# Performance work log

Hardware: AMD Instinct MI355X
Metric: run time of the kernel (lower is better)

Reference implementation:

```python
import jax, jax.numpy as jnp
import numpy as np

H = 128; W = 128; WH = 8; WW = 8; SH = 4; SW = 4
DIM = 512; HEADS = 16; HD = DIM // HEADS; HIDDEN = 2048
NH = H // WH; NW = W // WW; NWIN = NH * NW; WL = WH * WW
EPS = 1e-5
SCALE = HD ** -0.5


def _rel_pos_index():
    # Swin-style relative position index, static (WL, WL) int table
    coords = np.stack(np.meshgrid(np.arange(WH), np.arange(WW), indexing='ij')).reshape(2, -1)
    rel = (coords[:, :, None] - coords[:, None, :]).transpose(1, 2, 0)  # (WL, WL, 2)
    rel[:, :, 0] += WH - 1
    rel[:, :, 1] += WW - 1
    rel[:, :, 0] *= 2 * WW - 1
    return rel.sum(-1)  # (WL, WL), values in [0, (2WH-1)(2WW-1))


def _shift_attn_mask():
    # static shifted-window attention mask, (NWIN, WL, WL)
    m = np.zeros((H, W))
    cnt = 0
    for hs in (slice(0, -WH), slice(-WH, -SH), slice(-SH, None)):
        for ws in (slice(0, -WW), slice(-WW, -SW), slice(-SW, None)):
            m[hs, ws] = cnt
            cnt += 1
    mw = m.reshape(NH, WH, NW, WW).transpose(0, 2, 1, 3).reshape(NWIN, WL)
    am = mw[:, None, :] - mw[:, :, None]
    return np.where(am != 0, -100.0, 0.0).astype(np.float32)


_RPI = _rel_pos_index()
_MASK = _shift_attn_mask()


def _layernorm(x, w, b):
    mu = x.mean(-1, keepdims=True)
    var = ((x - mu) ** 2).mean(-1, keepdims=True)
    return (x - mu) / jnp.sqrt(var + EPS) * w + b


def _win_part(x):  # (H, W, D) -> (NWIN, WL, D)
    return x.reshape(NH, WH, NW, WW, DIM).transpose(0, 2, 1, 3, 4).reshape(NWIN, WL, DIM)


def _win_rev(w):  # (NWIN, WL, D) -> (H, W, D)
    return w.reshape(NH, NW, WH, WW, DIM).transpose(0, 2, 1, 3, 4).reshape(H, W, DIM)


def setup_inputs() -> dict:
    key = jax.random.key(0)
    ks = jax.random.split(key, 8)
    s = 0.02
    return {
        'x': jax.random.normal(ks[0], (H * W, DIM), dtype=jnp.float32),
        'ln1_w': jnp.ones((DIM,), jnp.float32),
        'ln1_b': jnp.zeros((DIM,), jnp.float32),
        'ln2_w': jnp.ones((DIM,), jnp.float32),
        'ln2_b': jnp.zeros((DIM,), jnp.float32),
        'qkv_w': jax.random.normal(ks[1], (3 * DIM, DIM), dtype=jnp.float32) * s,
        'qkv_b': jnp.zeros((3 * DIM,), jnp.float32),
        'proj_w': jax.random.normal(ks[2], (DIM, DIM), dtype=jnp.float32) * s,
        'proj_b': jnp.zeros((DIM,), jnp.float32),
        'rpb': jax.random.normal(ks[3], ((2 * WH - 1) * (2 * WW - 1), HEADS), dtype=jnp.float32) * s,
        'mlp_w1': jax.random.normal(ks[4], (HIDDEN, DIM), dtype=jnp.float32) * s,
        'mlp_b1': jnp.zeros((HIDDEN,), jnp.float32),
        'mlp_w2': jax.random.normal(ks[5], (DIM, HIDDEN), dtype=jnp.float32) * s,
        'mlp_b2': jnp.zeros((DIM,), jnp.float32),
    }


def reference(x, ln1_w, ln1_b, ln2_w, ln2_b, qkv_w, qkv_b, proj_w, proj_b, rpb,
              mlp_w1, mlp_b1, mlp_w2, mlp_b2):
    skip = x
    h = _layernorm(x, ln1_w, ln1_b).reshape(H, W, DIM)
    # cyclic shift + window partition
    h = jnp.roll(h, shift=(-SH, -SW), axis=(0, 1))
    xw = _win_part(h)  # (NWIN, WL, DIM)
    # windowed multi-head self-attention (equinox Linear: y = W @ x + b)
    qkv = jnp.einsum('nld,ed->nle', xw, qkv_w) + qkv_b
    q, k, v = [t.reshape(NWIN, WL, HEADS, HD).transpose(0, 2, 1, 3)
               for t in jnp.split(qkv, 3, axis=-1)]  # each (NWIN, HEADS, WL, HD)
    attn = jnp.einsum('nhqd,nhkd->nhqk', q * SCALE, k)
    bias = rpb[_RPI.reshape(-1)].reshape(WL, WL, HEADS).transpose(2, 0, 1)  # (HEADS, WL, WL)
    attn = attn + bias[None] + jnp.asarray(_MASK)[:, None]
    attn = jax.nn.softmax(attn, axis=-1)
    out = jnp.einsum('nhqk,nhkd->nhqd', attn, v).transpose(0, 2, 1, 3).reshape(NWIN, WL, DIM)
    out = jnp.einsum('nld,ed->nle', out, proj_w) + proj_b
    # window reverse + reverse cyclic shift
    h = jnp.roll(_win_rev(out), shift=(SH, SW), axis=(0, 1)).reshape(H * W, DIM)
    h = skip + h  # residual (drop_path is Identity at rate 0)
    # FFN branch (note: original code does x = x + drop_path(x), i.e. 2*mlp(norm2(.)))
    h = _layernorm(h, ln2_w, ln2_b)
    m = jax.nn.gelu(jnp.einsum('ld,ed->le', h, mlp_w1) + mlp_b1)
    m = jnp.einsum('le,de->ld', m, mlp_w2) + mlp_b2
    return m + m
```

## Files before the change

### kernel.cpp

```cpp
#include <hip/hip_runtime.h>
#include <hip/hip_bf16.h>
#include <stdint.h>

#define TOK   16384
#define DIMM  512
#define NHEAD 16
#define HDIM  32
#define HID   2048
#define NWIN  256
#define WLEN  64
#define EPSV  1e-5f
#define SCL   0.17677669529663687f

typedef __hip_bfloat16 bf16;
typedef __attribute__((ext_vector_type(8))) __bf16 bf16x8;
typedef __attribute__((ext_vector_type(4))) float f32x4;

__device__ __forceinline__ int remap_row(int r){
  int win = r >> 6, l = r & 63;
  int gh = ((win >> 4) << 3) + (l >> 3);
  int gw = ((win & 15) << 3) + (l & 7);
  int oh = (gh + 4) & 127, ow = (gw + 4) & 127;
  return (oh << 7) + ow;
}

__device__ __forceinline__ int region_of(int win, int l){
  int gh = ((win >> 4) << 3) + (l >> 3);
  int gw = ((win & 15) << 3) + (l & 7);
  int rh = (gh < 120) ? 0 : ((gh < 124) ? 1 : 2);
  int rw = (gw < 120) ? 0 : ((gw < 124) ? 1 : 2);
  return rh * 3 + rw;
}

__device__ __forceinline__ void gl_lds16(const bf16* g, bf16* l){
  __builtin_amdgcn_global_load_lds((const __attribute__((address_space(1))) void*)g,
                                   (__attribute__((address_space(3))) void*)l, 16, 0, 0);
}

__global__ __launch_bounds__(256) void convert_w(const float* __restrict__ a,
                                                 const float* __restrict__ b,
                                                 const float* __restrict__ c,
                                                 const float* __restrict__ d,
                                                 bf16* __restrict__ dst){
  int e = (blockIdx.x * 256 + threadIdx.x) * 4;
  float4 v;
  if (e < 786432)        v = *(const float4*)(a + e);
  else if (e < 1048576)  v = *(const float4*)(b + (e - 786432));
  else if (e < 2097152)  v = *(const float4*)(c + (e - 1048576));
  else                   v = *(const float4*)(d + (e - 2097152));
  union { bf16 h[4]; int2 q; } u;
  u.h[0] = __float2bfloat16(v.x); u.h[1] = __float2bfloat16(v.y);
  u.h[2] = __float2bfloat16(v.z); u.h[3] = __float2bfloat16(v.w);
  *(int2*)(dst + e) = u.q;
}

template<bool REMAP>
__global__ __launch_bounds__(256) void ln_kernel(const float* __restrict__ in,
    const float* __restrict__ w, const float* __restrict__ b, bf16* __restrict__ outp)
{
  const int wave = threadIdx.x >> 6, lane = threadIdx.x & 63;
  const int r = blockIdx.x * 4 + wave;
  const int src = REMAP ? remap_row(r) : r;
  const float4* row = (const float4*)(in + (size_t)src * DIMM);
  float4 v0 = row[lane*2], v1 = row[lane*2 + 1];
  float sm = v0.x+v0.y+v0.z+v0.w + v1.x+v1.y+v1.z+v1.w;
  float sq = v0.x*v0.x+v0.y*v0.y+v0.z*v0.z+v0.w*v0.w
           + v1.x*v1.x+v1.y*v1.y+v1.z*v1.z+v1.w*v1.w;
  #pragma unroll
  for (int off = 1; off < 64; off <<= 1){
    sm += __shfl_xor(sm, off);
    sq += __shfl_xor(sq, off);
  }
  const float mean = sm * (1.f/512.f);
  const float rstd = rsqrtf(sq*(1.f/512.f) - mean*mean + EPSV);
  const float4* wp = (const float4*)w; const float4* bp = (const float4*)b;
  float4 w0 = wp[lane*2], w1 = wp[lane*2+1], b0 = bp[lane*2], b1 = bp[lane*2+1];
  union { bf16 h[8]; int4 q; } u;
  u.h[0] = __float2bfloat16((v0.x-mean)*rstd*w0.x + b0.x);
  u.h[1] = __float2bfloat16((v0.y-mean)*rstd*w0.y + b0.y);
  u.h[2] = __float2bfloat16((v0.z-mean)*rstd*w0.z + b0.z);
  u.h[3] = __float2bfloat16((v0.w-mean)*rstd*w0.w + b0.w);
  u.h[4] = __float2bfloat16((v1.x-mean)*rstd*w1.x + b1.x);
  u.h[5] = __float2bfloat16((v1.y-mean)*rstd*w1.y + b1.y);
  u.h[6] = __float2bfloat16((v1.z-mean)*rstd*w1.z + b1.z);
  u.h[7] = __float2bfloat16((v1.w-mean)*rstd*w1.w + b1.w);
  *(int4*)(outp + (size_t)r*DIMM + lane*8) = u.q;
}

#define M_QKV  0
#define M_PROJ 1
#define M_MLP1 2
#define M_MLP2 3
#define M_PART 4

template<int MODE, int K>
__global__ __launch_bounds__(256) void gemm_bt(const bf16* __restrict__ A,
    const bf16* __restrict__ Wt, const float* __restrict__ bias,
    bf16* __restrict__ out_b, float* __restrict__ out_f, const float* __restrict__ skip)
{
  __shared__ bf16 lsA[2][128*32];
  __shared__ bf16 lsB[2][128*32];
  const int tid = threadIdx.x, wave = tid >> 6, lane = tid & 63;
  const int lrow = lane & 15, lgrp = lane >> 4;
  const int m0 = blockIdx.x * 128, n0 = blockIdx.y * 128;
  const int wr = (wave >> 1) * 64, wc = (wave & 1) * 64;

  f32x4 acc[4][4] = {};

  const bf16* Abase = A  + (size_t)m0 * K;
  const bf16* Bbase = Wt + (size_t)n0 * K;
  const int srow = tid >> 2;
  const int scol = (tid & 3) * 8;

  #define STAGE(kt, bf) { \
    gl_lds16(Abase + (size_t)(srow)      * K + (kt) + scol, lsA[bf] + wave*512); \
    gl_lds16(Abase + (size_t)(srow + 64) * K + (kt) + scol, lsA[bf] + 2048 + wave*512); \
    gl_lds16(Bbase + (size_t)(srow)      * K + (kt) + scol, lsB[bf] + wave*512); \
    gl_lds16(Bbase + (size_t)(srow + 64) * K + (kt) + scol, lsB[bf] + 2048 + wave*512); \
  }

  STAGE(0, 0);
  __syncthreads();
  int cur = 0;
  for (int kt = 0; kt < K; kt += 32){
    if (kt + 32 < K) STAGE(kt + 32, cur ^ 1);
    bf16x8 af[4], bfv[4];
    #pragma unroll
    for (int i = 0; i < 4; i++){
      af[i]  = *(const bf16x8*)(lsA[cur] + (wr + i*16 + lrow)*32 + lgrp*8);
      bfv[i] = *(const bf16x8*)(lsB[cur] + (wc + i*16 + lrow)*32 + lgrp*8);
    }
    #pragma unroll
    for (int i = 0; i < 4; i++)
      #pragma unroll
      for (int j = 0; j < 4; j++)
        acc[i][j] = __builtin_amdgcn_mfma_f32_16x16x32_bf16(af[i], bfv[j], acc[i][j], 0, 0, 0);
    __syncthreads();
    cur ^= 1;
  }
  #undef STAGE

  #pragma unroll
  for (int i = 0; i < 4; i++){
    #pragma unroll
    for (int j = 0; j < 4; j++){
      const int col   = n0 + wc + j*16 + lrow;
      const int row_b = m0 + wr + i*16 + lgrp*4;
      const float bv = bias[col];
      #pragma unroll
      for (int rr = 0; rr < 4; rr++){
        const int row = row_b + rr;
        float v = acc[i][j][rr] + bv;
        if constexpr (MODE == M_PROJ){
          const int o = remap_row(row);
          out_f[(size_t)o*DIMM + col] = v + skip[(size_t)o*DIMM + col];
        } else {
          out_f[(size_t)row*DIMM + col] = v;
        }
      }
    }
  }
}

template<int KSTR>
__device__ __forceinline__ void stage_ht(const bf16* __restrict__ P,
                                         int grow0, bf16* lbase, int tid, int kt){
  const int r = tid >> 3;
  const int c = ((tid & 7) ^ (r & 7)) * 8;
  const bf16* g = P + (size_t)(grow0 + r) * KSTR + kt * 64 + c;
  bf16* l = lbase + r * 64 + (tid & 7) * 8;
  gl_lds16(g, l);
  gl_lds16(g + (size_t)64 * KSTR, l + 4096);
}

template<int MODE, int KEXT, int KSTR = KEXT>
__global__ __launch_bounds__(512, 2) void gemm8_bt(const bf16* __restrict__ A,
    const bf16* __restrict__ Wt, const float* __restrict__ bias,
    bf16* __restrict__ out_b, float* __restrict__ out_f, float* __restrict__ out_f2)
{
  constexpr int NT = KEXT / 64;
  extern __shared__ bf16 lds[];
  bf16* As = lds;
  bf16* Bs = lds + 32768;
  const int tid = threadIdx.x;
  const int ln = tid & 63, wv = tid >> 6;
  const int lrow = ln & 15, lgrp = ln >> 4;
  const int swz = lrow & 7;
  const int wm = wv >> 2, wn = wv & 3;
  const int m0 = blockIdx.x * 256, n0 = blockIdx.y * 256;

  if constexpr (MODE == M_PART){
    const int z = blockIdx.z;
    A  += z * 1024;
    Wt += z * 1024;
  }

  f32x4 acc[8][4] = {};
  bf16x8 aA[4][2], bB0[2][2], bB1[2][2];

  #define LDA(MH) { _Pragma("unroll") for (int mf = 0; mf < 4; mf++) \
    _Pragma("unroll") for (int ks = 0; ks < 2; ks++) \
      aA[mf][ks] = *(const bf16x8*)(As + s*16384 + (wm*128 + (MH)*64 + mf*16 + lrow)*64 + ((ks*4 + lgrp) ^ swz)*8); }
  #define LDB(DST, NH) { _Pragma("unroll") for (int nf = 0; nf < 2; nf++) \
    _Pragma("unroll") for (int ks = 0; ks < 2; ks++) \
      DST[nf][ks] = *(const bf16x8*)(Bs + s*16384 + (wn*64 + (NH)*32 + nf*16 + lrow)*64 + ((ks*4 + lgrp) ^ swz)*8); }
  #define QUAD(BARR, IM0, JN0) { _Pragma("unroll") for (int ks = 0; ks < 2; ks++) \
    _Pragma("unroll") for (int mf = 0; mf < 4; mf++) \
      _Pragma("unroll") for (int nf = 0; nf < 2; nf++) \
        acc[(IM0)+mf][(JN0)+nf] = __builtin_amdgcn_mfma_f32_16x16x32_bf16(aA[mf][ks], BARR[nf][ks], acc[(IM0)+mf][(JN0)+nf], 0, 0, 0); }
  #define SBAR() { __builtin_amdgcn_sched_barrier(0); __builtin_amdgcn_s_barrier(); __builtin_amdgcn_sched_barrier(0); }
  #define LGKM0() { asm volatile("s_waitcnt lgkmcnt(0)" ::: "memory"); __builtin_amdgcn_sched_barrier(0); }

  stage_ht<KSTR>(A,  m0,       As,        tid, 0);
  stage_ht<KSTR>(Wt, n0,       Bs,        tid, 0);
  stage_ht<KSTR>(Wt, n0 + 128, Bs + 8192, tid, 0);
  stage_ht<KSTR>(A,  m0 + 128, As + 8192, tid, 0);
  asm volatile("s_waitcnt vmcnt(0)" ::: "memory");
  SBAR();
  stage_ht<KSTR>(Wt, n0,       Bs + 16384,        tid, 1);
  stage_ht<KSTR>(A,  m0,       As + 16384,        tid, 1);
  stage_ht<KSTR>(Wt, n0 + 128, Bs + 16384 + 8192, tid, 1);

  for (int t = 0; t < NT; ++t){
    const int s = t & 1;
    const int sx = s ^ 1;
    LDA(0); LDB(bB0, 0);
    if (t + 1 < NT) stage_ht<KSTR>(A, m0 + 128, As + sx*16384 + 8192, tid, t + 1);
    LGKM0();
    __builtin_amdgcn_s_setprio(1); QUAD(bB0, 0, 0); __builtin_amdgcn_s_setprio(0);
    SBAR();
    LDB(bB1, 1);
    LGKM0();
    __builtin_amdgcn_s_setprio(1); QUAD(bB1, 0, 2); __builtin_amdgcn_s_setprio(0);
    SBAR();
    LDA(1);
    if (t + 2 < NT) stage_ht<KSTR>(Wt, n0, Bs + s*16384, tid, t + 2);
    LGKM0();
    __builtin_amdgcn_s_setprio(1); QUAD(bB1, 4, 2); __builtin_amdgcn_s_setprio(0);
    SBAR();
    if (t + 2 < NT){
      stage_ht<KSTR>(A,  m0,       As + s*16384,        tid, t + 2);
      stage_ht<KSTR>(Wt, n0 + 128, Bs + s*16384 + 8192, tid, t + 2);
    }
    __builtin_amdgcn_s_setprio(1); QUAD(bB0, 4, 0); __builtin_amdgcn_s_setprio(0);
    if (t == NT - 2)      { asm volatile("s_waitcnt vmcnt(0)" ::: "memory"); }
    else if (t < NT - 2)  { asm volatile("s_waitcnt vmcnt(6)" ::: "memory"); }
    SBAR();
  }
  #undef LDA
  #undef LDB
  #undef QUAD
  #undef SBAR
  #undef LGKM0

  bf16* pdstb = nullptr;
  if constexpr (MODE == M_PART)
    pdstb = blockIdx.z ? (bf16*)out_f2 : (bf16*)out_f;
  #pragma unroll
  for (int im = 0; im < 8; im++){
    #pragma unroll
    for (int jn = 0; jn < 4; jn++){
      const int col = n0 + wn*64 + (jn >> 1)*32 + (jn & 1)*16 + lrow;
      const int row_b = m0 + wm*128 + (im >> 2)*64 + (im & 3)*16 + lgrp*4;
      const float bv = (MODE == M_PART) ? 0.f : bias[col];
      #pragma unroll
      for (int rr = 0; rr < 4; rr++){
        const int row = row_b + rr;
        float v = acc[im][jn][rr] + bv;
        if constexpr (MODE == M_QKV){
          const int t = col >> 9, rem = col & 511;
          const int head = rem >> 5, hd = rem & 31;
          const int win = row >> 6, l = row & 63;
          out_b[(size_t)t * (TOK*DIMM) + ((size_t)(win*NHEAD + head)*WLEN + l)*HDIM + hd]
              = __float2bfloat16(v);
        } else if constexpr (MODE == M_MLP1){
          const float u = 1.5957691216057308f * (v + 0.044715f*v*v*v);
          const float g = v * (1.0f / (1.0f + __expf(-u)));
          out_b[(size_t)row*HID + col] = __float2bfloat16(g);
        } else if constexpr (MODE == M_PART){
          pdstb[(size_t)row*DIMM + col] = __float2bfloat16(v);
        } else {
          out_f[(size_t)row*DIMM + col] = 2.f * v;
        }
      }
    }
  }
}

__global__ __launch_bounds__(256) void mlp2_reduce(const bf16* __restrict__ p0,
    const bf16* __restrict__ p1, float* __restrict__ dout, const float* __restrict__ bias){
  const size_t i = (size_t)(blockIdx.x * 256 + threadIdx.x) * 8;
  int4 a = *(const int4*)(p0 + i);
  int4 b = *(const int4*)(p1 + i);
  const int cb = (int)(i & 511);
  const float4 bv0 = *(const float4*)(bias + cb);
  const float4 bv1 = *(const float4*)(bias + cb + 4);
  const bf16* ah = (const bf16*)&a;
  const bf16* bh = (const bf16*)&b;
  float4 r0, r1;
  r0.x = 2.f*(__bfloat162float(ah[0]) + __bfloat162float(bh[0]) + bv0.x);
  r0.y = 2.f*(__bfloat162float(ah[1]) + __bfloat162float(bh[1]) + bv0.y);
  r0.z = 2.f*(__bfloat162float(ah[2]) + __bfloat162float(bh[2]) + bv0.z);
  r0.w = 2.f*(__bfloat162float(ah[3]) + __bfloat162float(bh[3]) + bv0.w);
  r1.x = 2.f*(__bfloat162float(ah[4]) + __bfloat162float(bh[4]) + bv1.x);
  r1.y = 2.f*(__bfloat162float(ah[5]) + __bfloat162float(bh[5]) + bv1.y);
  r1.z = 2.f*(__bfloat162float(ah[6]) + __bfloat162float(bh[6]) + bv1.z);
  r1.w = 2.f*(__bfloat162float(ah[7]) + __bfloat162float(bh[7]) + bv1.w);
  *(float4*)(dout + i)     = r0;
  *(float4*)(dout + i + 4) = r1;
}

__global__ __launch_bounds__(256) void attn_kernel(const bf16* __restrict__ qkv,
    const float* __restrict__ rpb, bf16* __restrict__ outp)
{
  __shared__ bf16 Pl[4][64][72];
  const int wave = threadIdx.x >> 6, lane = threadIdx.x & 63;
  const int lrow = lane & 15, lgrp = lane >> 4;
  const int wh = blockIdx.x * 4 + wave;
  const int win = wh >> 4, head = wh & 15;
  const bf16* qb = qkv + (size_t)wh * (WLEN*HDIM);
  const bf16* kb = qb + (size_t)TOK * DIMM;
  const bf16* vb = kb + (size_t)TOK * DIMM;

  bf16x8 aq[4], ak[4];
  #pragma unroll
  for (int i = 0; i < 4; i++){
    aq[i] = *(const bf16x8*)(qb + (i*16 + lrow)*HDIM + lgrp*8);
    ak[i] = *(const bf16x8*)(kb + (i*16 + lrow)*HDIM + lgrp*8);
  }
  f32x4 s[4][4] = {};
  #pragma unroll
  for (int i = 0; i < 4; i++)
    #pragma unroll
    for (int j = 0; j < 4; j++)
      s[i][j] = __builtin_amdgcn_mfma_f32_16x16x32_bf16(aq[i], ak[j], s[i][j], 0, 0, 0);

  #pragma unroll
  for (int i = 0; i < 4; i++){
    #pragma unroll
    for (int rr = 0; rr < 4; rr++){
      const int srow = i*16 + lgrp*4 + rr;
      const int rq = region_of(win, srow);
      float vals[4]; float mx = -1e30f;
      #pragma unroll
      for (int j = 0; j < 4; j++){
        const int scol = j*16 + lrow;
        const int idx = ((srow>>3) - (scol>>3) + 7)*15 + ((srow&7) - (scol&7) + 7);
        float v = s[i][j][rr]*SCL + rpb[idx*NHEAD + head];
        if (region_of(win, scol) != rq) v -= 100.f;
        vals[j] = v; mx = fmaxf(mx, v);
      }
      mx = fmaxf(mx, __shfl_xor(mx, 1));
      mx = fmaxf(mx, __shfl_xor(mx, 2));
      mx = fmaxf(mx, __shfl_xor(mx, 4));
      mx = fmaxf(mx, __shfl_xor(mx, 8));
      float sum = 0.f;
      #pragma unroll
      for (int j = 0; j < 4; j++){ vals[j] = __expf(vals[j] - mx); sum += vals[j]; }
      sum += __shfl_xor(sum, 1); sum += __shfl_xor(sum, 2);
      sum += __shfl_xor(sum, 4); sum += __shfl_xor(sum, 8);
      const float rs = 1.f / sum;
      #pragma unroll
      for (int j = 0; j < 4; j++)
        Pl[wave][srow][j*16 + lrow] = __float2bfloat16(vals[j] * rs);
    }
  }

  f32x4 o[4][2] = {};
  const __bf16* vraw = (const __bf16*)vb;
  #pragma unroll
  for (int st = 0; st < 2; st++){
    bf16x8 pa[4];
    #pragma unroll
    for (int i = 0; i < 4; i++)
      pa[i] = *(const bf16x8*)(&Pl[wave][i*16 + lrow][st*32 + lgrp*8]);
    bf16x8 bv[2];
    #pragma unroll
    for (int j = 0; j < 2; j++){
      #pragma unroll
      for (int jj = 0; jj < 8; jj++)
        bv[j][jj] = vraw[(size_t)(st*32 + lgrp*8 + jj)*HDIM + j*16 + lrow];
    }
    #pragma unroll
    for (int i = 0; i < 4; i++)
      #pragma unroll
      for (int j = 0; j < 2; j++)
        o[i][j] = __builtin_amdgcn_mfma_f32_16x16x32_bf16(pa[i], bv[j], o[i][j], 0, 0, 0);
  }
  bf16* orow = outp + (size_t)win * WLEN * DIMM + head * HDIM;
  #pragma unroll
  for (int i = 0; i < 4; i++)
    #pragma unroll
    for (int j = 0; j < 2; j++)
      #pragma unroll
      for (int rr = 0; rr < 4; rr++){
        const int l = i*16 + lgrp*4 + rr;
        orow[(size_t)l * DIMM + j*16 + lrow] = __float2bfloat16(o[i][j][rr]);
      }
}

extern "C" void kernel_launch(void* const* d_in, const int* in_sizes, int n_in,
                              void* d_out, int out_size, void* d_ws, size_t ws_size,
                              hipStream_t stream) {
  const float* x     = (const float*)d_in[0];
  const float* ln1w  = (const float*)d_in[1];
  const float* ln1b  = (const float*)d_in[2];
  const float* ln2w  = (const float*)d_in[3];
  const float* ln2b  = (const float*)d_in[4];
  const float* qkvw  = (const float*)d_in[5];
  const float* qkvbi = (const float*)d_in[6];
  const float* projw = (const float*)d_in[7];
  const float* projb = (const float*)d_in[8];
  const float* rpb   = (const float*)d_in[9];
  const float* m1w   = (const float*)d_in[10];
  const float* m1b   = (const float*)d_in[11];
  const float* m2w   = (const float*)d_in[12];
  const float* m2b   = (const float*)d_in[13];

  bf16* wqkv  = (bf16*)d_ws;
  bf16* wproj = wqkv + 786432;
  bf16* wm1   = wproj + 262144;
  bf16* wm2   = wm1 + 1048576;
  bf16* xw    = wm2 + 1048576;
  float* hbuf = (float*)(xw + 8388608);
  bf16* qkvb  = (bf16*)(hbuf + 8388608);
  bf16* attno = qkvb + 3*(size_t)8388608;
  bf16* m1buf = qkvb;
  bf16* h2    = xw;

  hipFuncSetAttribute((const void*)&gemm8_bt<M_QKV, 512>,
                      hipFuncAttributeMaxDynamicSharedMemorySize, 131072);
  hipFuncSetAttribute((const void*)&gemm8_bt<M_MLP1, 512>,
                      hipFuncAttributeMaxDynamicSharedMemorySize, 131072);
  hipFuncSetAttribute((const void*)&gemm8_bt<M_PART, 1024, 2048>,
                      hipFuncAttributeMaxDynamicSharedMemorySize, 131072);

  convert_w<<<3072, 256, 0, stream>>>(qkvw, projw, m1w, m2w, wqkv);
  ln_kernel<true><<<4096, 256, 0, stream>>>(x, ln1w, ln1b, xw);
  { dim3 g(TOK/256, 1536/256);
    gemm8_bt<M_QKV, 512><<<g, 512, 131072, stream>>>(xw, wqkv, qkvbi, qkvb, nullptr, nullptr); }
  attn_kernel<<<1024, 256, 0, stream>>>(qkvb, rpb, attno);
  { dim3 g(TOK/128, 512/128);
    gemm_bt<M_PROJ, 512><<<g, 256, 0, stream>>>(attno, wproj, projb, nullptr, hbuf, x); }
  ln_kernel<false><<<4096, 256, 0, stream>>>(hbuf, ln2w, ln2b, h2);
  { dim3 g(TOK/256, 2048/256);
    gemm8_bt<M_MLP1, 512><<<g, 512, 131072, stream>>>(h2, wm1, m1b, m1buf, nullptr, nullptr); }
  { dim3 g(TOK/256, 512/256, 2);
    gemm8_bt<M_PART, 1024, 2048><<<g, 512, 131072, stream>>>(m1buf, wm2, m2b, nullptr,
                                                             (float*)hbuf, (float*)xw); }
  mlp2_reduce<<<8388608/8/256, 256, 0, stream>>>((const bf16*)hbuf, (const bf16*)xw,
                                                 (float*)d_out, m2b);
}
```

Measured before the change: 222.6 us.

## Restructure GEMM main loop into two phases with full A fragments in registers

The bf16 MFMA GEMM loop now loads both A halves into registers at once and issues each B half's MFMAs back to back. This cuts the per-K-tile schedule from four barrier-separated quadrant phases to two, and drops the explicit lgkmcnt waits. Global-to-LDS staging is reorganised so B is prefetched one tile ahead and A two tiles ahead, with the vmcnt threshold adjusted to match. Launch bounds drop to one block per CU, giving each thread more registers for the extra fragments. The cost is weaker overlap from fewer phases and a dependence on the new prefetch ordering being race-free.

```diff
diff --git a/kernel.cpp b/kernel.cpp
--- a/kernel.cpp
+++ b/kernel.cpp
@@ -174,7 +174,7 @@
 }
 
 template<int MODE, int KEXT, int KSTR = KEXT>
-__global__ __launch_bounds__(512, 2) void gemm8_bt(const bf16* __restrict__ A,
+__global__ __launch_bounds__(512, 1) void gemm8_bt(const bf16* __restrict__ A,
     const bf16* __restrict__ Wt, const float* __restrict__ bias,
     bf16* __restrict__ out_b, float* __restrict__ out_f, float* __restrict__ out_f2)
 {
@@ -190,26 +190,24 @@
   const int m0 = blockIdx.x * 256, n0 = blockIdx.y * 256;
 
   if constexpr (MODE == M_PART){
-    const int z = blockIdx.z;
-    A  += z * 1024;
-    Wt += z * 1024;
+    A  += blockIdx.z * 1024;
+    Wt += blockIdx.z * 1024;
   }
 
   f32x4 acc[8][4] = {};
-  bf16x8 aA[4][2], bB0[2][2], bB1[2][2];
-
-  #define LDA(MH) { _Pragma("unroll") for (int mf = 0; mf < 4; mf++) \
+  bf16x8 aA0[4][2], aA1[4][2], bB0[2][2], bB1[2][2];
+
+  #define LDA(DST, MH) { _Pragma("unroll") for (int mf = 0; mf < 4; mf++) \
     _Pragma("unroll") for (int ks = 0; ks < 2; ks++) \
-      aA[mf][ks] = *(const bf16x8*)(As + s*16384 + (wm*128 + (MH)*64 + mf*16 + lrow)*64 + ((ks*4 + lgrp) ^ swz)*8); }
+      DST[mf][ks] = *(const bf16x8*)(As + s*16384 + (wm*128 + (MH)*64 + mf*16 + lrow)*64 + ((ks*4 + lgrp) ^ swz)*8); }
   #define LDB(DST, NH) { _Pragma("unroll") for (int nf = 0; nf < 2; nf++) \
     _Pragma("unroll") for (int ks = 0; ks < 2; ks++) \
       DST[nf][ks] = *(const bf16x8*)(Bs + s*16384 + (wn*64 + (NH)*32 + nf*16 + lrow)*64 + ((ks*4 + lgrp) ^ swz)*8); }
-  #define QUAD(BARR, IM0, JN0) { _Pragma("unroll") for (int ks = 0; ks < 2; ks++) \
+  #define QUAD(AR, BR, IM0, JN0) { _Pragma("unroll") for (int ks = 0; ks < 2; ks++) \
     _Pragma("unroll") for (int mf = 0; mf < 4; mf++) \
       _Pragma("unroll") for (int nf = 0; nf < 2; nf++) \
-        acc[(IM0)+mf][(JN0)+nf] = __builtin_amdgcn_mfma_f32_16x16x32_bf16(aA[mf][ks], BARR[nf][ks], acc[(IM0)+mf][(JN0)+nf], 0, 0, 0); }
+        acc[(IM0)+mf][(JN0)+nf] = __builtin_amdgcn_mfma_f32_16x16x32_bf16(AR[mf][ks], BR[nf][ks], acc[(IM0)+mf][(JN0)+nf], 0, 0, 0); }
   #define SBAR() { __builtin_amdgcn_sched_barrier(0); __builtin_amdgcn_s_barrier(); __builtin_amdgcn_sched_barrier(0); }
-  #define LGKM0() { asm volatile("s_waitcnt lgkmcnt(0)" ::: "memory"); __builtin_amdgcn_sched_barrier(0); }
 
   stage_ht<KSTR>(A,  m0,       As,        tid, 0);
   stage_ht<KSTR>(Wt, n0,       Bs,        tid, 0);
@@ -217,41 +215,39 @@
   stage_ht<KSTR>(A,  m0 + 128, As + 8192, tid, 0);
   asm volatile("s_waitcnt vmcnt(0)" ::: "memory");
   SBAR();
-  stage_ht<KSTR>(Wt, n0,       Bs + 16384,        tid, 1);
-  stage_ht<KSTR>(A,  m0,       As + 16384,        tid, 1);
-  stage_ht<KSTR>(Wt, n0 + 128, Bs + 16384 + 8192, tid, 1);
+  stage_ht<KSTR>(A, m0,       As + 16384,        tid, 1);
+  stage_ht<KSTR>(A, m0 + 128, As + 16384 + 8192, tid, 1);
 
   for (int t = 0; t < NT; ++t){
     const int s = t & 1;
     const int sx = s ^ 1;
-    LDA(0); LDB(bB0, 0);
-    if (t + 1 < NT) stage_ht<KSTR>(A, m0 + 128, As + sx*16384 + 8192, tid, t + 1);
-    LGKM0();
-    __builtin_amdgcn_s_setprio(1); QUAD(bB0, 0, 0); __builtin_amdgcn_s_setprio(0);
+    LDA(aA0, 0); LDB(bB0, 0); LDA(aA1, 1);
+    if (t + 1 < NT){
+      stage_ht<KSTR>(Wt, n0,       Bs + sx*16384,        tid, t + 1);
+      stage_ht<KSTR>(Wt, n0 + 128, Bs + sx*16384 + 8192, tid, t + 1);
+    }
+    __builtin_amdgcn_s_setprio(1);
+    QUAD(aA0, bB0, 0, 0);
+    QUAD(aA1, bB0, 4, 0);
+    __builtin_amdgcn_s_setprio(0);
     SBAR();
     LDB(bB1, 1);
-    LGKM0();
-    __builtin_amdgcn_s_setprio(1); QUAD(bB1, 0, 2); __builtin_amdgcn_s_setprio(0);
-    SBAR();
-    LDA(1);
-    if (t + 2 < NT) stage_ht<KSTR>(Wt, n0, Bs + s*16384, tid, t + 2);
-    LGKM0();
-    __builtin_amdgcn_s_setprio(1); QUAD(bB1, 4, 2); __builtin_amdgcn_s_setprio(0);
-    SBAR();
     if (t + 2 < NT){
-      stage_ht<KSTR>(A,  m0,       As + s*16384,        tid, t + 2);
-      stage_ht<KSTR>(Wt, n0 + 128, Bs + s*16384 + 8192, tid, t + 2);
-    }
-    __builtin_amdgcn_s_setprio(1); QUAD(bB0, 4, 0); __builtin_amdgcn_s_setprio(0);
+      stage_ht<KSTR>(A, m0,       As + s*16384,        tid, t + 2);
+      stage_ht<KSTR>(A, m0 + 128, As + s*16384 + 8192, tid, t + 2);
+    }
+    __builtin_amdgcn_s_setprio(1);
+    QUAD(aA0, bB1, 0, 2);
+    QUAD(aA1, bB1, 4, 2);
+    __builtin_amdgcn_s_setprio(0);
     if (t == NT - 2)      { asm volatile("s_waitcnt vmcnt(0)" ::: "memory"); }
-    else if (t < NT - 2)  { asm volatile("s_waitcnt vmcnt(6)" ::: "memory"); }
+    else if (t < NT - 2)  { asm volatile("s_waitcnt vmcnt(4)" ::: "memory"); }
     SBAR();
   }
   #undef LDA
   #undef LDB
   #undef QUAD
   #undef SBAR
-  #undef LGKM0
 
   bf16* pdstb = nullptr;
   if constexpr (MODE == M_PART)
```

New measurement: 223.1 us. Within noise of the previous version (+0.2%).
